# Kernel tuning notes

Hardware: AMD Instinct MI355X
Metric: run time of the kernel (lower is better)

## Reference

```python
import jax, jax.numpy as jnp
import numpy as np

EMBED = 1024
HEADS = 16
HEAD_DIM = EMBED // HEADS


def setup_inputs() -> dict:
    key = jax.random.key(0)
    ks = jax.random.split(key, 8)
    N, S = 4, 2048
    return {
        "keys": jax.random.normal(ks[0], (N, S, EMBED), dtype=jnp.float32),
        "query": jax.random.normal(ks[1], (N, S, EMBED), dtype=jnp.float32),
        "values": jax.random.normal(ks[2], (N, S, EMBED), dtype=jnp.float32),
        "Wk": jax.random.normal(ks[3], (HEAD_DIM, HEAD_DIM), dtype=jnp.float32) / np.sqrt(HEAD_DIM),
        "Wq": jax.random.normal(ks[4], (HEAD_DIM, HEAD_DIM), dtype=jnp.float32) / np.sqrt(HEAD_DIM),
        "Wv": jax.random.normal(ks[5], (HEAD_DIM, HEAD_DIM), dtype=jnp.float32) / np.sqrt(HEAD_DIM),
        "Wo": jax.random.normal(ks[6], (EMBED, EMBED), dtype=jnp.float32) / np.sqrt(EMBED),
        "bo": jax.random.normal(ks[7], (EMBED,), dtype=jnp.float32) * 0.01,
    }


def reference(keys, query, values, Wk, Wq, Wv, Wo, bo):
    N, Q, _ = query.shape
    K = keys.shape[1]
    # split heads: [n, s, h, d]
    k = keys.reshape(N, K, HEADS, HEAD_DIM) @ Wk.T
    q = query.reshape(N, Q, HEADS, HEAD_DIM) @ Wq.T
    v = values.reshape(N, K, HEADS, HEAD_DIM) @ Wv.T
    energy = jnp.einsum("nqhd,nkhd->nhqk", q, k)
    # NOTE: original torch code scales by embed_size**1 / 2 == embed_size/2 (quirk, kept faithful)
    attention = jax.nn.softmax(energy / (EMBED / 2), axis=3)
    out = jnp.einsum("nhqk,nkhd->nqhd", attention, v).reshape(N, Q, EMBED)
    return out @ Wo.T + bo
```

## Files before the change

kernel.cpp:

```cpp
#include <hip/hip_runtime.h>
#include <hip/hip_bf16.h>

#define HEADS 16
#define HDIM 64
#define EMB 1024
#define NBATCH 4
#define SEQ 2048
#define NT (SEQ/64)

typedef __bf16 bf16x8 __attribute__((ext_vector_type(8)));
typedef __bf16 bf16x4 __attribute__((ext_vector_type(4)));
typedef float f32x4 __attribute__((ext_vector_type(4)));
typedef float f32x16 __attribute__((ext_vector_type(16)));

#define Z16 {0.f,0.f,0.f,0.f,0.f,0.f,0.f,0.f,0.f,0.f,0.f,0.f,0.f,0.f,0.f,0.f}

static __device__ __forceinline__ bf16x8 load_cvt8(const float* __restrict__ p) {
    float4 a = *reinterpret_cast<const float4*>(p);
    float4 b = *reinterpret_cast<const float4*>(p + 4);
    bf16x8 r;
    r[0] = (__bf16)a.x; r[1] = (__bf16)a.y; r[2] = (__bf16)a.z; r[3] = (__bf16)a.w;
    r[4] = (__bf16)b.x; r[5] = (__bf16)b.y; r[6] = (__bf16)b.z; r[7] = (__bf16)b.w;
    return r;
}

static __device__ __forceinline__ unsigned cvt_pk_bf16(float a, float b) {
    unsigned d;
    asm("v_cvt_pk_bf16_f32 %0, %1, %2" : "=v"(d) : "v"(a), "v"(b));
    return d;
}

static __device__ __forceinline__ void pl_swap(unsigned &a, unsigned &b) {
#if __has_builtin(__builtin_amdgcn_permlane32_swap)
    auto r = __builtin_amdgcn_permlane32_swap((int)a, (int)b, false, false);
    a = (unsigned)r[0]; b = (unsigned)r[1];
#else
    asm("v_permlane32_swap_b32 %0, %1" : "+v"(a), "+v"(b));
#endif
}

__global__ __launch_bounds__(256) void proj_kernel(
    const float* __restrict__ keys, const float* __restrict__ query,
    const float* __restrict__ values,
    const float* __restrict__ Wk, const float* __restrict__ Wq,
    const float* __restrict__ Wv, const float* __restrict__ Wo,
    __bf16* __restrict__ qb, __bf16* __restrict__ kb, __bf16* __restrict__ vtb,
    __bf16* __restrict__ wob)
{
    int t = threadIdx.x;
    int which = blockIdx.z;

    if (which == 3) {
        int idx = blockIdx.y*gridDim.x + blockIdx.x;
        if (idx < EMB*EMB/4/256) {
            int i = idx*256 + t;
            float4 v = reinterpret_cast<const float4*>(Wo)[i];
            bf16x4 r;
            r[0] = (__bf16)v.x; r[1] = (__bf16)v.y; r[2] = (__bf16)v.z; r[3] = (__bf16)v.w;
            reinterpret_cast<bf16x4*>(wob)[i] = r;
        }
        return;
    }

    __shared__ __align__(16) __bf16 vlds[64][72];

    int wave = t >> 6, lane = t & 63;
    int l16 = lane & 15, g = lane >> 4;
    int sblk = blockIdx.x, nh = blockIdx.y;
    int n = nh >> 4, h = nh & 15;

    const float* X = (which == 0) ? query : (which == 1) ? keys : values;
    const float* W = (which == 0) ? Wq    : (which == 1) ? Wk   : Wv;
    const float wsc = (which == 0) ? (1.44269504088896f / 512.f) : 1.0f;

    {
        const float* wp = W + t*16;
        int row = t >> 2, c0 = (t & 3)*16;
#pragma unroll
        for (int q4 = 0; q4 < 4; ++q4) {
            float4 v = *reinterpret_cast<const float4*>(wp + q4*4);
            vlds[row][c0 + q4*4 + 0] = (__bf16)(v.x*wsc);
            vlds[row][c0 + q4*4 + 1] = (__bf16)(v.y*wsc);
            vlds[row][c0 + q4*4 + 2] = (__bf16)(v.z*wsc);
            vlds[row][c0 + q4*4 + 3] = (__bf16)(v.w*wsc);
        }
    }
    __syncthreads();

    bf16x8 wf[4][2];
#pragma unroll
    for (int j = 0; j < 4; ++j)
#pragma unroll
        for (int kc = 0; kc < 2; ++kc)
            wf[j][kc] = *reinterpret_cast<const bf16x8*>(&vlds[j*16 + l16][kc*32 + g*8]);

    int s0 = sblk*64 + wave*16;
    const float* xp = X + ((size_t)(n*SEQ + s0 + l16)*HEADS + h)*64;
    bf16x8 af0 = load_cvt8(xp + g*8);
    bf16x8 af1 = load_cvt8(xp + 32 + g*8);

    __syncthreads();

    f32x4 acc[4];
#pragma unroll
    for (int j = 0; j < 4; ++j) acc[j] = (f32x4){0.f, 0.f, 0.f, 0.f};
#pragma unroll
    for (int j = 0; j < 4; ++j) {
        acc[j] = __builtin_amdgcn_mfma_f32_16x16x32_bf16(af0, wf[j][0], acc[j], 0, 0, 0);
        acc[j] = __builtin_amdgcn_mfma_f32_16x16x32_bf16(af1, wf[j][1], acc[j], 0, 0, 0);
    }

#pragma unroll
    for (int j = 0; j < 4; ++j)
#pragma unroll
        for (int r = 0; r < 4; ++r)
            vlds[wave*16 + g*4 + r][j*16 + l16] = (__bf16)acc[j][r];
    __syncthreads();

    if (which < 2) {
        int row = t >> 2, seg = t & 3;
        __bf16* dst = (which == 0 ? qb : kb) + (size_t)nh*SEQ*64
                      + (size_t)(sblk*64 + row)*64 + seg*16;
        *reinterpret_cast<int4*>(dst)     = *reinterpret_cast<const int4*>(&vlds[row][seg*16]);
        *reinterpret_cast<int4*>(dst + 8) = *reinterpret_cast<const int4*>(&vlds[row][seg*16 + 8]);
    } else {
        int d = t & 63, sc4 = t >> 6;
        alignas(16) __bf16 tmp[16];
#pragma unroll
        for (int i = 0; i < 16; ++i) tmp[i] = vlds[sc4*16 + i][d];
        __bf16* dst = vtb + ((size_t)nh*64 + d)*SEQ + sblk*64 + sc4*16;
        *reinterpret_cast<int4*>(dst)     = *reinterpret_cast<const int4*>(tmp);
        *reinterpret_cast<int4*>(dst + 8) = *reinterpret_cast<const int4*>(tmp + 8);
    }
}

__global__ __launch_bounds__(256, 2) void attn_kernel(
    const __bf16* __restrict__ qb, const __bf16* __restrict__ kb,
    const __bf16* __restrict__ vtb, __bf16* __restrict__ ob)
{
    __shared__ __align__(16) char smem[65536];

    int t = threadIdx.x;
    int wave = t >> 6, lane = t & 63;
    int l31 = lane & 31, hi = lane >> 5;

    int id = blockIdx.x;
    int qblk = id >> 6;
    int nh = (id & 7)*8 + ((id >> 3) & 7);
    int n = nh >> 4, h = nh & 15;

    const __bf16* Qp = qb  + (size_t)nh*SEQ*64;
    const __bf16* Kp = kb  + (size_t)nh*SEQ*64;
    const __bf16* Vp = vtb + (size_t)nh*64*SEQ;

    int st_row[2], st_col[2];
#pragma unroll
    for (int i = 0; i < 2; ++i) {
        int o = wave*2048 + i*1024 + lane*16;
        st_row[i] = o >> 7;
        st_col[i] = (o & 127) ^ ((st_row[i] & 7) << 4);
    }

    int q0 = qblk*256 + wave*64;
    const __bf16* qp = Qp + (size_t)(q0 + l31)*64 + hi*8;
    bf16x8 qfA[4], qfB[4];
#pragma unroll
    for (int i = 0; i < 4; ++i) {
        qfA[i] = *reinterpret_cast<const bf16x8*>(qp + i*16);
        qfB[i] = *reinterpret_cast<const bf16x8*>(qp + 2048 + i*16);
    }

    f32x16 oaccA0 = Z16, oaccA1 = Z16, oaccB0 = Z16, oaccB1 = Z16;
    float lsA0 = 0.f, lsA1 = 0.f, lsA2 = 0.f, lsA3 = 0.f;
    float lsB0 = 0.f, lsB1 = 0.f, lsB2 = 0.f, lsB3 = 0.f;

#define STAGE_TILE(gbase, stride, ldsoff)                                          \
    {                                                                              \
        _Pragma("unroll")                                                          \
        for (int i_ = 0; i_ < 2; ++i_) {                                           \
            const char* g_ = (const char*)((gbase) + (size_t)st_row[i_]*(stride))  \
                             + st_col[i_];                                         \
            __builtin_amdgcn_global_load_lds(                                      \
                (const __attribute__((address_space(1))) void*)g_,                 \
                (__attribute__((address_space(3))) void*)(smem + (ldsoff)          \
                    + wave*2048 + i_*1024), 16, 0, 0);                             \
        }                                                                          \
    }

#define QKT2()                                                                     \
    {                                                                              \
        bf16x8 k00_ = *(const bf16x8*)(kb_ + (l31)*128      + ((0*32 + hi*16) ^ swz)); \
        bf16x8 k01_ = *(const bf16x8*)(kb_ + (l31)*128      + ((1*32 + hi*16) ^ swz)); \
        bf16x8 k02_ = *(const bf16x8*)(kb_ + (l31)*128      + ((2*32 + hi*16) ^ swz)); \
        bf16x8 k03_ = *(const bf16x8*)(kb_ + (l31)*128      + ((3*32 + hi*16) ^ swz)); \
        bf16x8 k10_ = *(const bf16x8*)(kb_ + (32 + l31)*128 + ((0*32 + hi*16) ^ swz)); \
        bf16x8 k11_ = *(const bf16x8*)(kb_ + (32 + l31)*128 + ((1*32 + hi*16) ^ swz)); \
        bf16x8 k12_ = *(const bf16x8*)(kb_ + (32 + l31)*128 + ((2*32 + hi*16) ^ swz)); \
        bf16x8 k13_ = *(const bf16x8*)(kb_ + (32 + l31)*128 + ((3*32 + hi*16) ^ swz)); \
        eA0 = __builtin_amdgcn_mfma_f32_32x32x16_bf16(k00_, qfA[0], eA0, 0, 0, 0); \
        eB0 = __builtin_amdgcn_mfma_f32_32x32x16_bf16(k00_, qfB[0], eB0, 0, 0, 0); \
        eA1 = __builtin_amdgcn_mfma_f32_32x32x16_bf16(k10_, qfA[0], eA1, 0, 0, 0); \
        eB1 = __builtin_amdgcn_mfma_f32_32x32x16_bf16(k10_, qfB[0], eB1, 0, 0, 0); \
        eA0 = __builtin_amdgcn_mfma_f32_32x32x16_bf16(k01_, qfA[1], eA0, 0, 0, 0); \
        eB0 = __builtin_amdgcn_mfma_f32_32x32x16_bf16(k01_, qfB[1], eB0, 0, 0, 0); \
        eA1 = __builtin_amdgcn_mfma_f32_32x32x16_bf16(k11_, qfA[1], eA1, 0, 0, 0); \
        eB1 = __builtin_amdgcn_mfma_f32_32x32x16_bf16(k11_, qfB[1], eB1, 0, 0, 0); \
        eA0 = __builtin_amdgcn_mfma_f32_32x32x16_bf16(k02_, qfA[2], eA0, 0, 0, 0); \
        eB0 = __builtin_amdgcn_mfma_f32_32x32x16_bf16(k02_, qfB[2], eB0, 0, 0, 0); \
        eA1 = __builtin_amdgcn_mfma_f32_32x32x16_bf16(k12_, qfA[2], eA1, 0, 0, 0); \
        eB1 = __builtin_amdgcn_mfma_f32_32x32x16_bf16(k12_, qfB[2], eB1, 0, 0, 0); \
        eA0 = __builtin_amdgcn_mfma_f32_32x32x16_bf16(k03_, qfA[3], eA0, 0, 0, 0); \
        eB0 = __builtin_amdgcn_mfma_f32_32x32x16_bf16(k03_, qfB[3], eB0, 0, 0, 0); \
        eA1 = __builtin_amdgcn_mfma_f32_32x32x16_bf16(k13_, qfA[3], eA1, 0, 0, 0); \
        eB1 = __builtin_amdgcn_mfma_f32_32x32x16_bf16(k13_, qfB[3], eB1, 0, 0, 0); \
    }

#define MAKE_PU_FAST(E, P, PU0, PU1)                                               \
    {                                                                              \
        _Pragma("unroll")                                                          \
        for (int i_ = 0; i_ < 16; ++i_)                                            \
            P[i_] = __builtin_amdgcn_exp2f(E[i_]);                                 \
        unsigned w00 = cvt_pk_bf16(P[0],  P[1]);                                   \
        unsigned w01 = cvt_pk_bf16(P[2],  P[3]);                                   \
        unsigned w10 = cvt_pk_bf16(P[4],  P[5]);                                   \
        unsigned w11 = cvt_pk_bf16(P[6],  P[7]);                                   \
        unsigned w20 = cvt_pk_bf16(P[8],  P[9]);                                   \
        unsigned w21 = cvt_pk_bf16(P[10], P[11]);                                  \
        unsigned w30 = cvt_pk_bf16(P[12], P[13]);                                  \
        unsigned w31 = cvt_pk_bf16(P[14], P[15]);                                  \
        pl_swap(w00, w10); pl_swap(w01, w11);                                      \
        pl_swap(w20, w30); pl_swap(w21, w31);                                      \
        PU0.u[0] = w00; PU0.u[1] = w01; PU0.u[2] = w10; PU0.u[3] = w11;            \
        PU1.u[0] = w20; PU1.u[1] = w21; PU1.u[2] = w30; PU1.u[3] = w31;            \
    }

#define LS_ACC(P, LS0, LS1, LS2, LS3)                                              \
    {                                                                              \
        LS0 += P[0] + P[4];  LS1 += P[1] + P[5];                                   \
        LS2 += P[2] + P[6];  LS3 += P[3] + P[7];                                   \
        LS0 += P[8] + P[12]; LS1 += P[9] + P[13];                                  \
        LS2 += P[10] + P[14]; LS3 += P[11] + P[15];                                \
    }

#define SMPV(SB, EA, EB)                                                           \
    {                                                                              \
        union { unsigned u[4]; bf16x8 v; } puA0, puA1, puB0, puB1;                 \
        float pA_[16], pB_[16];                                                    \
        MAKE_PU_FAST(EA, pA_, puA0, puA1)                                          \
        MAKE_PU_FAST(EB, pB_, puB0, puB1)                                          \
        bf16x8 v00 = *(const bf16x8*)(vb_ + (l31)*128      + (((SB)*64 +  0 + hi*16) ^ swz)); \
        bf16x8 v01 = *(const bf16x8*)(vb_ + (l31)*128      + (((SB)*64 + 32 + hi*16) ^ swz)); \
        bf16x8 v10 = *(const bf16x8*)(vb_ + (32 + l31)*128 + (((SB)*64 +  0 + hi*16) ^ swz)); \
        bf16x8 v11 = *(const bf16x8*)(vb_ + (32 + l31)*128 + (((SB)*64 + 32 + hi*16) ^ swz)); \
        oaccA0 = __builtin_amdgcn_mfma_f32_32x32x16_bf16(v00, puA0.v, oaccA0, 0, 0, 0); \
        oaccA1 = __builtin_amdgcn_mfma_f32_32x32x16_bf16(v10, puA0.v, oaccA1, 0, 0, 0); \
        oaccB0 = __builtin_amdgcn_mfma_f32_32x32x16_bf16(v00, puB0.v, oaccB0, 0, 0, 0); \
        oaccB1 = __builtin_amdgcn_mfma_f32_32x32x16_bf16(v10, puB0.v, oaccB1, 0, 0, 0); \
        oaccA0 = __builtin_amdgcn_mfma_f32_32x32x16_bf16(v01, puA1.v, oaccA0, 0, 0, 0); \
        oaccA1 = __builtin_amdgcn_mfma_f32_32x32x16_bf16(v11, puA1.v, oaccA1, 0, 0, 0); \
        oaccB0 = __builtin_amdgcn_mfma_f32_32x32x16_bf16(v01, puB1.v, oaccB0, 0, 0, 0); \
        oaccB1 = __builtin_amdgcn_mfma_f32_32x32x16_bf16(v11, puB1.v, oaccB1, 0, 0, 0); \
        LS_ACC(pA_, lsA0, lsA1, lsA2, lsA3)                                        \
        LS_ACC(pB_, lsB0, lsB1, lsB2, lsB3)                                        \
    }

    STAGE_TILE(Kp, 64, 0);
    STAGE_TILE(Vp, SEQ, 32768);
    STAGE_TILE(Kp + (size_t)64*64, 64, 8192);
    STAGE_TILE(Vp + 64, SEQ, 32768 + 8192);

    for (int kt = 0; kt < NT; ++kt) {
        if (kt + 2 < NT) {
            int b2 = (kt + 2) & 3;
            const __bf16* knext = Kp + (size_t)(kt + 2)*64*64;
            const __bf16* vnext = Vp + (size_t)(kt + 2)*64;
            STAGE_TILE(knext, 64, b2*8192);
            STAGE_TILE(vnext, SEQ, 32768 + b2*8192);
        }
        if (kt < NT - 2)       asm volatile("s_waitcnt vmcnt(8)" ::: "memory");
        else if (kt == NT - 2) asm volatile("s_waitcnt vmcnt(4)" ::: "memory");
        else                   asm volatile("s_waitcnt vmcnt(0)" ::: "memory");
        __builtin_amdgcn_s_barrier();
        __builtin_amdgcn_sched_barrier(0);

        const char* kb_ = smem + (kt & 3)*8192;
        const char* vb_ = smem + 32768 + (kt & 3)*8192;
        int swz = (l31 & 7) << 4;

        f32x16 eA0 = Z16, eB0 = Z16, eA1 = Z16, eB1 = Z16;
        QKT2()
        SMPV(0, eA0, eB0)
        SMPV(1, eA1, eB1)
    }

    float lA = (lsA0 + lsA1) + (lsA2 + lsA3);
    float totA = lA + __shfl_xor(lA, 32);
    float invA = 1.f / totA;
    float lB = (lsB0 + lsB1) + (lsB2 + lsB3);
    float totB = lB + __shfl_xor(lB, 32);
    float invB = 1.f / totB;

    __bf16* opA = ob + (size_t)(n*SEQ + q0 + l31)*EMB + h*64;
    __bf16* opB = opA + (size_t)32*EMB;
#pragma unroll
    for (int j = 0; j < 4; ++j)
#pragma unroll
        for (int c = 0; c < 4; ++c) {
            int d_ = c + 8*j + 4*hi;
            opA[d_]      = (__bf16)(oaccA0[4*j + c] * invA);
            opA[32 + d_] = (__bf16)(oaccA1[4*j + c] * invA);
            opB[d_]      = (__bf16)(oaccB0[4*j + c] * invB);
            opB[32 + d_] = (__bf16)(oaccB1[4*j + c] * invB);
        }
#undef STAGE_TILE
#undef QKT2
#undef MAKE_PU_FAST
#undef LS_ACC
#undef SMPV
}

__global__ __launch_bounds__(256, 2) void out_gemm_kernel(
    const __bf16* __restrict__ ob, const __bf16* __restrict__ wob,
    const float* __restrict__ bo, float* __restrict__ out)
{
    __shared__ __align__(16) char smem[65536];

    int t = threadIdx.x;
    int wave = t >> 6, lane = t & 63;
    int l16 = lane & 15, g = lane >> 4;

    int bid = blockIdx.x;
    int swz = (bid & 7)*64 + (bid >> 3);
    int mb = (swz >> 3)*128;
    int nb = (swz & 7)*128;
    int wr = wave >> 1, wc = wave & 1;

    int st_row[4], st_col[4];
#pragma unroll
    for (int i = 0; i < 4; ++i) {
        int o = i*4096 + wave*1024 + lane*16;
        st_row[i] = o >> 7;
        st_col[i] = (o & 127) ^ ((st_row[i] & 7) << 4);
    }

#define G_STAGE(kt, buf)                                                            \
    {                                                                               \
        _Pragma("unroll")                                                           \
        for (int i_ = 0; i_ < 4; ++i_) {                                            \
            const char* ga_ = (const char*)(ob + (size_t)(mb + st_row[i_])*EMB      \
                                + (kt)*64) + st_col[i_];                            \
            __builtin_amdgcn_global_load_lds(                                       \
                (const __attribute__((address_space(1))) void*)ga_,                 \
                (__attribute__((address_space(3))) void*)(smem + (buf)*16384        \
                    + i_*4096 + wave*1024), 16, 0, 0);                              \
            const char* gb_ = (const char*)(wob + (size_t)(nb + st_row[i_])*EMB     \
                                + (kt)*64) + st_col[i_];                            \
            __builtin_amdgcn_global_load_lds(                                       \
                (const __attribute__((address_space(1))) void*)gb_,                 \
                (__attribute__((address_space(3))) void*)(smem + 32768 + (buf)*16384\
                    + i_*4096 + wave*1024), 16, 0, 0);                              \
        }                                                                           \
    }

    f32x4 acc[4][4];
#pragma unroll
    for (int m = 0; m < 4; ++m)
#pragma unroll
        for (int n = 0; n < 4; ++n) acc[m][n] = (f32x4){0.f, 0.f, 0.f, 0.f};

    G_STAGE(0, 0);
    __syncthreads();

    int cur = 0;
    for (int kt = 0; kt < EMB/64; ++kt) {
        if (kt + 1 < EMB/64) G_STAGE(kt + 1, cur ^ 1);

        const char* ab_ = smem + cur*16384;
        const char* bb_ = smem + 32768 + cur*16384;

        bf16x8 af[4][2], bf[4][2];
#pragma unroll
        for (int m = 0; m < 4; ++m) {
            int row = wr*64 + m*16 + l16, s = (row & 7) << 4;
            af[m][0] = *(const bf16x8*)(ab_ + row*128 + ((g*16) ^ s));
            af[m][1] = *(const bf16x8*)(ab_ + row*128 + ((64 + g*16) ^ s));
        }
#pragma unroll
        for (int n = 0; n < 4; ++n) {
            int row = wc*64 + n*16 + l16, s = (row & 7) << 4;
            bf[n][0] = *(const bf16x8*)(bb_ + row*128 + ((g*16) ^ s));
            bf[n][1] = *(const bf16x8*)(bb_ + row*128 + ((64 + g*16) ^ s));
        }

        __builtin_amdgcn_s_setprio(1);
#pragma unroll
        for (int m = 0; m < 4; ++m)
#pragma unroll
            for (int n = 0; n < 4; ++n) {
                acc[m][n] = __builtin_amdgcn_mfma_f32_16x16x32_bf16(af[m][0], bf[n][0], acc[m][n], 0, 0, 0);
                acc[m][n] = __builtin_amdgcn_mfma_f32_16x16x32_bf16(af[m][1], bf[n][1], acc[m][n], 0, 0, 0);
            }
        __builtin_amdgcn_s_setprio(0);

        __syncthreads();
        cur ^= 1;
    }

#pragma unroll
    for (int n = 0; n < 4; ++n) {
        int col = nb + wc*64 + n*16 + l16;
        float bias = bo[col];
#pragma unroll
        for (int m = 0; m < 4; ++m) {
            int rowb = mb + wr*64 + m*16 + g*4;
#pragma unroll
            for (int r = 0; r < 4; ++r)
                out[(size_t)(rowb + r)*EMB + col] = acc[m][n][r] + bias;
        }
    }
#undef G_STAGE
}

extern "C" void kernel_launch(void* const* d_in, const int* in_sizes, int n_in,
                              void* d_out, int out_size, void* d_ws, size_t ws_size,
                              hipStream_t stream) {
    const float* keys   = (const float*)d_in[0];
    const float* query  = (const float*)d_in[1];
    const float* values = (const float*)d_in[2];
    const float* Wk     = (const float*)d_in[3];
    const float* Wq     = (const float*)d_in[4];
    const float* Wv     = (const float*)d_in[5];
    const float* Wo     = (const float*)d_in[6];
    const float* bo     = (const float*)d_in[7];
    float* out = (float*)d_out;

    char* ws = (char*)d_ws;
    __bf16* qb  = (__bf16*)(ws);
    __bf16* kb  = (__bf16*)(ws + (size_t)16*1024*1024);
    __bf16* vtb = (__bf16*)(ws + (size_t)32*1024*1024);
    __bf16* ob  = (__bf16*)(ws + (size_t)48*1024*1024);
    __bf16* wob = (__bf16*)(ws + (size_t)64*1024*1024);

    hipLaunchKernelGGL(proj_kernel, dim3(SEQ/64, NBATCH*HEADS, 4), dim3(256), 0, stream,
                       keys, query, values, Wk, Wq, Wv, Wo, qb, kb, vtb, wob);
    hipLaunchKernelGGL(attn_kernel, dim3(512), dim3(256), 0, stream,
                       qb, kb, vtb, ob);
    hipLaunchKernelGGL(out_gemm_kernel, dim3(512), dim3(256), 0, stream,
                       ob, wob, bo, out);
}
```

Baseline: 124.2 us.

## Software-pipeline QK^T across KV tiles to overlap with softmax and PV

Restructures the attention main loop so the QK^T MFMAs for the next half-tile (including the first half of the next KV tile) are issued between the softmax/PV stages of the current tile. The loop is unrolled by two with ping-pong energy accumulators, plus a prologue and epilogue. The aim is to hide the exp/convert latency of softmax behind independent matrix work and keep the MFMA units busy. The cost is higher register pressure from the extra live accumulators, and the next tile's K must already be resident in LDS, which the existing 2-ahead staging provides.

Measured after the change: 122.8 us. About the same (-1.1%).

```diff
diff --git a/kernel.cpp b/kernel.cpp
--- a/kernel.cpp
+++ b/kernel.cpp
@@ -174,6 +174,9 @@
     float lsA0 = 0.f, lsA1 = 0.f, lsA2 = 0.f, lsA3 = 0.f;
     float lsB0 = 0.f, lsB1 = 0.f, lsB2 = 0.f, lsB3 = 0.f;
 
+    const char* vb_;
+    int swz = (l31 & 7) << 4;
+
 #define STAGE_TILE(gbase, stride, ldsoff)                                          \
     {                                                                              \
         _Pragma("unroll")                                                          \
@@ -187,32 +190,27 @@
         }                                                                          \
     }
 
-#define QKT2()                                                                     \
-    {                                                                              \
-        bf16x8 k00_ = *(const bf16x8*)(kb_ + (l31)*128      + ((0*32 + hi*16) ^ swz)); \
-        bf16x8 k01_ = *(const bf16x8*)(kb_ + (l31)*128      + ((1*32 + hi*16) ^ swz)); \
-        bf16x8 k02_ = *(const bf16x8*)(kb_ + (l31)*128      + ((2*32 + hi*16) ^ swz)); \
-        bf16x8 k03_ = *(const bf16x8*)(kb_ + (l31)*128      + ((3*32 + hi*16) ^ swz)); \
-        bf16x8 k10_ = *(const bf16x8*)(kb_ + (32 + l31)*128 + ((0*32 + hi*16) ^ swz)); \
-        bf16x8 k11_ = *(const bf16x8*)(kb_ + (32 + l31)*128 + ((1*32 + hi*16) ^ swz)); \
-        bf16x8 k12_ = *(const bf16x8*)(kb_ + (32 + l31)*128 + ((2*32 + hi*16) ^ swz)); \
-        bf16x8 k13_ = *(const bf16x8*)(kb_ + (32 + l31)*128 + ((3*32 + hi*16) ^ swz)); \
-        eA0 = __builtin_amdgcn_mfma_f32_32x32x16_bf16(k00_, qfA[0], eA0, 0, 0, 0); \
-        eB0 = __builtin_amdgcn_mfma_f32_32x32x16_bf16(k00_, qfB[0], eB0, 0, 0, 0); \
-        eA1 = __builtin_amdgcn_mfma_f32_32x32x16_bf16(k10_, qfA[0], eA1, 0, 0, 0); \
-        eB1 = __builtin_amdgcn_mfma_f32_32x32x16_bf16(k10_, qfB[0], eB1, 0, 0, 0); \
-        eA0 = __builtin_amdgcn_mfma_f32_32x32x16_bf16(k01_, qfA[1], eA0, 0, 0, 0); \
-        eB0 = __builtin_amdgcn_mfma_f32_32x32x16_bf16(k01_, qfB[1], eB0, 0, 0, 0); \
-        eA1 = __builtin_amdgcn_mfma_f32_32x32x16_bf16(k11_, qfA[1], eA1, 0, 0, 0); \
-        eB1 = __builtin_amdgcn_mfma_f32_32x32x16_bf16(k11_, qfB[1], eB1, 0, 0, 0); \
-        eA0 = __builtin_amdgcn_mfma_f32_32x32x16_bf16(k02_, qfA[2], eA0, 0, 0, 0); \
-        eB0 = __builtin_amdgcn_mfma_f32_32x32x16_bf16(k02_, qfB[2], eB0, 0, 0, 0); \
-        eA1 = __builtin_amdgcn_mfma_f32_32x32x16_bf16(k12_, qfA[2], eA1, 0, 0, 0); \
-        eB1 = __builtin_amdgcn_mfma_f32_32x32x16_bf16(k12_, qfB[2], eB1, 0, 0, 0); \
-        eA0 = __builtin_amdgcn_mfma_f32_32x32x16_bf16(k03_, qfA[3], eA0, 0, 0, 0); \
-        eB0 = __builtin_amdgcn_mfma_f32_32x32x16_bf16(k03_, qfB[3], eB0, 0, 0, 0); \
-        eA1 = __builtin_amdgcn_mfma_f32_32x32x16_bf16(k13_, qfA[3], eA1, 0, 0, 0); \
-        eB1 = __builtin_amdgcn_mfma_f32_32x32x16_bf16(k13_, qfB[3], eB1, 0, 0, 0); \
+#define STAGE(s)                                                                   \
+    {                                                                              \
+        int b_ = (s) & 3;                                                          \
+        STAGE_TILE(Kp + (size_t)(s)*64*64, 64, b_*8192);                           \
+        STAGE_TILE(Vp + (size_t)(s)*64, SEQ, 32768 + b_*8192);                     \
+    }
+
+#define QKTH(KBP, RO, EA, EB)                                                      \
+    {                                                                              \
+        bf16x8 kf0_ = *(const bf16x8*)((KBP) + ((RO) + l31)*128 + ((0*32 + hi*16) ^ swz)); \
+        bf16x8 kf1_ = *(const bf16x8*)((KBP) + ((RO) + l31)*128 + ((1*32 + hi*16) ^ swz)); \
+        bf16x8 kf2_ = *(const bf16x8*)((KBP) + ((RO) + l31)*128 + ((2*32 + hi*16) ^ swz)); \
+        bf16x8 kf3_ = *(const bf16x8*)((KBP) + ((RO) + l31)*128 + ((3*32 + hi*16) ^ swz)); \
+        EA = __builtin_amdgcn_mfma_f32_32x32x16_bf16(kf0_, qfA[0], EA, 0, 0, 0);   \
+        EB = __builtin_amdgcn_mfma_f32_32x32x16_bf16(kf0_, qfB[0], EB, 0, 0, 0);   \
+        EA = __builtin_amdgcn_mfma_f32_32x32x16_bf16(kf1_, qfA[1], EA, 0, 0, 0);   \
+        EB = __builtin_amdgcn_mfma_f32_32x32x16_bf16(kf1_, qfB[1], EB, 0, 0, 0);   \
+        EA = __builtin_amdgcn_mfma_f32_32x32x16_bf16(kf2_, qfA[2], EA, 0, 0, 0);   \
+        EB = __builtin_amdgcn_mfma_f32_32x32x16_bf16(kf2_, qfB[2], EB, 0, 0, 0);   \
+        EA = __builtin_amdgcn_mfma_f32_32x32x16_bf16(kf3_, qfA[3], EA, 0, 0, 0);   \
+        EB = __builtin_amdgcn_mfma_f32_32x32x16_bf16(kf3_, qfB[3], EB, 0, 0, 0);   \
     }
 
 #define MAKE_PU_FAST(E, P, PU0, PU1)                                               \
@@ -264,33 +262,49 @@
         LS_ACC(pB_, lsB0, lsB1, lsB2, lsB3)                                        \
     }
 
-    STAGE_TILE(Kp, 64, 0);
-    STAGE_TILE(Vp, SEQ, 32768);
-    STAGE_TILE(Kp + (size_t)64*64, 64, 8192);
-    STAGE_TILE(Vp + 64, SEQ, 32768 + 8192);
-
-    for (int kt = 0; kt < NT; ++kt) {
-        if (kt + 2 < NT) {
-            int b2 = (kt + 2) & 3;
-            const __bf16* knext = Kp + (size_t)(kt + 2)*64*64;
-            const __bf16* vnext = Vp + (size_t)(kt + 2)*64;
-            STAGE_TILE(knext, 64, b2*8192);
-            STAGE_TILE(vnext, SEQ, 32768 + b2*8192);
-        }
-        if (kt < NT - 2)       asm volatile("s_waitcnt vmcnt(8)" ::: "memory");
-        else if (kt == NT - 2) asm volatile("s_waitcnt vmcnt(4)" ::: "memory");
-        else                   asm volatile("s_waitcnt vmcnt(0)" ::: "memory");
+#define BODY(T, XA, XB, ZA, ZB, DO_STAGE, VMN)                                     \
+    {                                                                              \
+        if (DO_STAGE) STAGE((T) + 2);                                              \
+        asm volatile("s_waitcnt vmcnt(" #VMN ")" ::: "memory");                    \
+        __builtin_amdgcn_s_barrier();                                              \
+        __builtin_amdgcn_sched_barrier(0);                                         \
+        const char* kcur_ = smem + ((T) & 3)*8192;                                 \
+        const char* knxt_ = smem + (((T) + 1) & 3)*8192;                           \
+        vb_ = smem + 32768 + ((T) & 3)*8192;                                       \
+        f32x16 yA_ = Z16, yB_ = Z16;                                               \
+        QKTH(kcur_, 32, yA_, yB_)                                                  \
+        SMPV(0, XA, XB)                                                            \
+        ZA = Z16; ZB = Z16;                                                        \
+        QKTH(knxt_, 0, ZA, ZB)                                                     \
+        SMPV(1, yA_, yB_)                                                          \
+    }
+
+    STAGE(0);
+    STAGE(1);
+    asm volatile("s_waitcnt vmcnt(4)" ::: "memory");
+    __builtin_amdgcn_s_barrier();
+    __builtin_amdgcn_sched_barrier(0);
+    f32x16 xA = Z16, xB = Z16;
+    f32x16 zA, zB;
+    QKTH(smem + 0, 0, xA, xB)
+
+    for (int p = 0; p < 15; ++p) {
+        int t0 = 2*p;
+        BODY(t0,     xA, xB, zA, zB, 1, 4)
+        BODY(t0 + 1, zA, zB, xA, xB, 1, 4)
+    }
+    BODY(30, xA, xB, zA, zB, 0, 0)
+
+    {
+        asm volatile("s_waitcnt vmcnt(0)" ::: "memory");
         __builtin_amdgcn_s_barrier();
         __builtin_amdgcn_sched_barrier(0);
-
-        const char* kb_ = smem + (kt & 3)*8192;
-        const char* vb_ = smem + 32768 + (kt & 3)*8192;
-        int swz = (l31 & 7) << 4;
-
-        f32x16 eA0 = Z16, eB0 = Z16, eA1 = Z16, eB1 = Z16;
-        QKT2()
-        SMPV(0, eA0, eB0)
-        SMPV(1, eA1, eB1)
+        const char* kcur_ = smem + (31 & 3)*8192;
+        vb_ = smem + 32768 + (31 & 3)*8192;
+        f32x16 yA_ = Z16, yB_ = Z16;
+        QKTH(kcur_, 32, yA_, yB_)
+        SMPV(0, zA, zB)
+        SMPV(1, yA_, yB_)
     }
 
     float lA = (lsA0 + lsA1) + (lsA2 + lsA3);
@@ -313,10 +327,12 @@
             opB[32 + d_] = (__bf16)(oaccB1[4*j + c] * invB);
         }
 #undef STAGE_TILE
-#undef QKT2
+#undef STAGE
+#undef QKTH
 #undef MAKE_PU_FAST
 #undef LS_ACC
 #undef SMPV
+#undef BODY
 }
 
 __global__ __launch_bounds__(256, 2) void out_gemm_kernel(
```
